# Kernel optimization log

Hardware: AMD Instinct MI355X
Metric: run time of the kernel (lower is better)

## Reference

```python
import jax, jax.numpy as jnp
import numpy as np

N = 50000
E = 800000
FEAT = 128
HID = 128
HEADS = 8
HEAD_DIM = HID // HEADS  # 16
NEG_SLOPE = 0.2


def _gat_layer(x, W, a_src, a_dst, b, src, dst, num_nodes):
    # x: [N, Fin]; W: [Fin, H*C]; a_src/a_dst: [H, C]; b: [H*C]
    H, C = a_src.shape
    h = (x @ W).reshape(num_nodes, H, C)               # [N,H,C]
    alpha_s = jnp.einsum('nhc,hc->nh', h, a_src)       # [N,H]
    alpha_d = jnp.einsum('nhc,hc->nh', h, a_dst)       # [N,H]
    e = jax.nn.leaky_relu(alpha_s[src] + alpha_d[dst], NEG_SLOPE)  # [E,H]
    # segment softmax over destination nodes (every node has a self-loop)
    m = jax.ops.segment_max(e, dst, num_segments=num_nodes)
    e = jnp.exp(e - m[dst])
    s = jax.ops.segment_sum(e, dst, num_segments=num_nodes)
    alpha = e / (s[dst] + 1e-16)                       # [E,H]
    msg = alpha[:, :, None] * h[src]                   # [E,H,C]
    out = jax.ops.segment_sum(msg, dst, num_segments=num_nodes)
    return out.reshape(num_nodes, H * C) + b


def setup_inputs() -> dict:
    key = jax.random.key(0)
    ks = jax.random.split(key, 12)
    x = jax.random.normal(ks[0], (N, FEAT), dtype=jnp.float32)
    edge_index = jax.random.randint(ks[1], (2, E), 0, N, dtype=jnp.int32)
    glorot = lambda k, shape: jax.random.uniform(
        k, shape, jnp.float32,
        -jnp.sqrt(6.0 / (shape[-2] + shape[-1])),
        jnp.sqrt(6.0 / (shape[-2] + shape[-1])))
    W1 = glorot(ks[2], (FEAT, HID))
    a_src1 = glorot(ks[3], (HEADS, HEAD_DIM))
    a_dst1 = glorot(ks[4], (HEADS, HEAD_DIM))
    b1 = jnp.zeros((HID,), jnp.float32)
    W2 = glorot(ks[5], (HID, HID))
    a_src2 = glorot(ks[6], (HEADS, HEAD_DIM))
    a_dst2 = glorot(ks[7], (HEADS, HEAD_DIM))
    b2 = jnp.zeros((HID,), jnp.float32)
    return {"x": x, "edge_index": edge_index,
            "W1": W1, "a_src1": a_src1, "a_dst1": a_dst1, "b1": b1,
            "W2": W2, "a_src2": a_src2, "a_dst2": a_dst2, "b2": b2}


def reference(x, edge_index, W1, a_src1, a_dst1, b1, W2, a_src2, a_dst2, b2):
    # GATConv adds self-loops to the (dense_to_sparse-derived) edge list
    loops = jnp.arange(N, dtype=edge_index.dtype)
    src = jnp.concatenate([edge_index[0], loops])
    dst = jnp.concatenate([edge_index[1], loops])
    h = _gat_layer(x, W1, a_src1, a_dst1, b1, src, dst, N)
    h = jax.nn.elu(h)
    # dropout: inference mode (training=False) -> identity
    h = _gat_layer(h, W2, a_src2, a_dst2, b2, src, dst, N)
    return jax.nn.elu(h)
```

## Files before the change

### kernel.cpp

```cpp
#include <hip/hip_runtime.h>
#include <hip/hip_fp16.h>
#include <math.h>

#define DEGMAX 64
#define CHUNK  2048
#define CAPB   6144

typedef _Float16 half8 __attribute__((ext_vector_type(8)));
typedef float    f32x4 __attribute__((ext_vector_type(4)));

__global__ __launch_bounds__(256) void k_csr(
        const int* __restrict__ gcur, const unsigned* __restrict__ bstore,
        int N, int* __restrict__ cnt, int* __restrict__ offs,
        unsigned short* __restrict__ adj) {
    int b = blockIdx.x;
    int t = threadIdx.x;
    int n0 = b << 8;
    int nb = N - n0; if (nb > 256) nb = 256;
    int ecnt = gcur[b]; if (ecnt > CAPB) ecnt = CAPB;
    __shared__ int lcnt[256], lofs[256], wsum[4];
    __shared__ unsigned short stage[CAPB];
    const unsigned* bp = bstore + (size_t)b * CAPB;

    lcnt[t] = 0;
    __syncthreads();
    for (int i = t; i < ecnt; i += 256)
        atomicAdd(&lcnt[bp[i] >> 16], 1);
    __syncthreads();
    int mycnt = lcnt[t];
    int lane = t & 63, wv = t >> 6;
    int x = mycnt;
    #pragma unroll
    for (int d = 1; d < 64; d <<= 1) {
        int y = __shfl_up(x, d);
        if (lane >= d) x += y;
    }
    if (lane == 63) wsum[wv] = x;
    __syncthreads();
    int base = 0;
    for (int k = 0; k < wv; k++) base += wsum[k];
    int myofs = base + x - mycnt;
    lofs[t] = myofs;
    if (t < nb) {
        cnt[n0 + t]  = mycnt;
        offs[n0 + t] = b * CAPB + myofs;
    }
    __syncthreads();
    lcnt[t] = 0;
    __syncthreads();
    for (int i = t; i < ecnt; i += 256) {
        unsigned p = bp[i];
        int node = p >> 16;
        int r = atomicAdd(&lcnt[node], 1);
        stage[lofs[node] + r] = (unsigned short)(p & 0xffffu);
    }
    __syncthreads();
    for (int i = t; i < ecnt; i += 256)
        adj[(size_t)b * CAPB + i] = stage[i];
}

__global__ void k_wcast(const float* __restrict__ W1, const float* __restrict__ as1,
                        const float* __restrict__ ad1, __half* __restrict__ Wf1,
                        const float* __restrict__ W2, const float* __restrict__ as2,
                        const float* __restrict__ ad2, __half* __restrict__ Wf2,
                        int* __restrict__ gcur) {
    int t = threadIdx.x;
    if (blockIdx.x == 0) gcur[t] = 0;
    int id2 = blockIdx.x * 256 + t;
    if (id2 >= 4608) return;
    int layer = id2 >= 2304 ? 1 : 0;
    const float* W  = layer ? W2  : W1;
    const float* av_s = layer ? as2 : as1;
    const float* av_d = layer ? ad2 : ad1;
    __half* Wf = layer ? Wf2 : Wf1;
    int id = id2 - layer * 2304;
    int lane = id & 63;
    int ct = (id >> 6) % 9;
    int kc = id / 576;
    int q = lane >> 4, n = lane & 15;
    #pragma unroll
    for (int j = 0; j < 8; j++) {
        int k = kc * 32 + q * 8 + j;
        float val;
        if (ct < 8) {
            val = W[(size_t)k * 128 + ct * 16 + n];
        } else {
            int h = n & 7;
            const float* a = (n < 8) ? av_s : av_d;
            float s = 0.f;
            #pragma unroll
            for (int c = 0; c < 16; c++)
                s += W[(size_t)k * 128 + h * 16 + c] * a[h * 16 + c];
            val = s;
        }
        Wf[(size_t)id * 8 + j] = __float2half(val);
    }
}

__device__ inline float4 ld4f(const float* p) { return *(const float4*)p; }

template<typename InT>
__device__ __forceinline__ void gemm_body(
        const InT* __restrict__ X, const __half* __restrict__ Wfrag,
        __half* __restrict__ H16, float* __restrict__ as_out,
        float* __restrict__ ad_out, int M, int bid) {
    __shared__ __half xls[64][136];
    int t = threadIdx.x;
    int w = t >> 6, lane = t & 63;
    int q = lane >> 4, n = lane & 15;
    int row0 = bid * 64;

    half8 bfrag[4][2];
    #pragma unroll
    for (int kc = 0; kc < 4; kc++)
        #pragma unroll
        for (int c2 = 0; c2 < 2; c2++) {
            int ct = w * 2 + c2;
            uint4 u = *(const uint4*)(Wfrag + (((size_t)(kc * 9 + ct)) * 64 + lane) * 8);
            bfrag[kc][c2] = *(half8*)&u;
        }
    half8 bfa[4];
    if (w == 0) {
        #pragma unroll
        for (int kc = 0; kc < 4; kc++) {
            uint4 u = *(const uint4*)(Wfrag + (((size_t)(kc * 9 + 8)) * 64 + lane) * 8);
            bfa[kc] = *(half8*)&u;
        }
    }

    #pragma unroll
    for (int rep = 0; rep < 8; rep++) {
        int lin = rep * 1024 + t * 4;
        int r = lin >> 7, k = lin & 127;
        int gr = row0 + r;
        uint2 u;
        if constexpr (sizeof(InT) == 4) {
            float4 v = (gr < M) ? ld4f((const float*)&X[(size_t)gr * 128 + k])
                                : make_float4(0.f, 0.f, 0.f, 0.f);
            __half2 h0 = __floats2half2_rn(v.x, v.y);
            __half2 h1 = __floats2half2_rn(v.z, v.w);
            u = make_uint2(*(unsigned*)&h0, *(unsigned*)&h1);
        } else {
            u = (gr < M) ? *(const uint2*)&X[(size_t)gr * 128 + k] : make_uint2(0, 0);
        }
        *(uint2*)&xls[r][k] = u;
    }
    __syncthreads();

    f32x4 acc[4][2], acca[4];
    #pragma unroll
    for (int rt = 0; rt < 4; rt++) {
        acc[rt][0] = (f32x4){0.f, 0.f, 0.f, 0.f};
        acc[rt][1] = (f32x4){0.f, 0.f, 0.f, 0.f};
        acca[rt]   = (f32x4){0.f, 0.f, 0.f, 0.f};
    }

    #pragma unroll
    for (int kc = 0; kc < 4; kc++)
        #pragma unroll
        for (int rt = 0; rt < 4; rt++) {
            uint4 au = *(const uint4*)&xls[rt * 16 + n][kc * 32 + q * 8];
            half8 af = *(half8*)&au;
            acc[rt][0] = __builtin_amdgcn_mfma_f32_16x16x32_f16(af, bfrag[kc][0], acc[rt][0], 0, 0, 0);
            acc[rt][1] = __builtin_amdgcn_mfma_f32_16x16x32_f16(af, bfrag[kc][1], acc[rt][1], 0, 0, 0);
            if (w == 0)
                acca[rt] = __builtin_amdgcn_mfma_f32_16x16x32_f16(af, bfa[kc], acca[rt], 0, 0, 0);
        }

    #pragma unroll
    for (int c2 = 0; c2 < 2; c2++) {
        int h = w * 2 + c2;
        #pragma unroll
        for (int rt = 0; rt < 4; rt++)
            #pragma unroll
            for (int reg = 0; reg < 4; reg++) {
                int grow = row0 + rt * 16 + q * 4 + reg;
                if (grow < M)
                    H16[(size_t)grow * 128 + h * 16 + n] = __float2half(acc[rt][c2][reg]);
            }
    }
    if (w == 0) {
        float* aout = (n < 8) ? as_out : ad_out;
        int h = n & 7;
        #pragma unroll
        for (int rt = 0; rt < 4; rt++)
            #pragma unroll
            for (int reg = 0; reg < 4; reg++) {
                int grow = row0 + rt * 16 + q * 4 + reg;
                if (grow < M) aout[grow * 8 + h] = acca[rt][reg];
            }
    }
}

__global__ __launch_bounds__(256) void k_bin_gemm(
        const float* __restrict__ X, const __half* __restrict__ Wfrag,
        __half* __restrict__ H16, float* __restrict__ as_out,
        float* __restrict__ ad_out, int M, int Gg,
        const int* __restrict__ src, const int* __restrict__ dst, int E, int K,
        int* __restrict__ gcur, unsigned* __restrict__ bstore) {
    int bid = blockIdx.x;
    if (bid < Gg) {
        gemm_body<float>(X, Wfrag, H16, as_out, ad_out, M, bid);
        return;
    }
    __shared__ int lcnt[256];
    __shared__ int gbase[256];
    int t = threadIdx.x;
    if (t < K) lcnt[t] = 0;
    __syncthreads();
    int e0 = (bid - Gg) * CHUNK;
    unsigned pk[8]; short bk[8], rk[8];
    #pragma unroll
    for (int j = 0; j < 8; j++) {
        int e = e0 + t + j * 256;
        bool v = e < E;
        int s = v ? src[e] : 0;
        int d = v ? dst[e] : 0;
        int b = d >> 8;
        pk[j] = ((unsigned)(d & 255) << 16) | (unsigned)s;
        bk[j] = (short)b;
        rk[j] = v ? (short)atomicAdd(&lcnt[b], 1) : (short)-1;
    }
    __syncthreads();
    if (t < K) gbase[t] = lcnt[t] ? atomicAdd(&gcur[t], lcnt[t]) : 0;
    __syncthreads();
    #pragma unroll
    for (int j = 0; j < 8; j++) {
        if (rk[j] >= 0) {
            int b = bk[j];
            int pos = gbase[b] + rk[j];
            if (pos < CAPB) bstore[(size_t)b * CAPB + pos] = pk[j];
        }
    }
}

__global__ __launch_bounds__(256) void k_gemm_mfma_h(
        const __half* __restrict__ X, const __half* __restrict__ Wfrag,
        __half* __restrict__ H16, float* __restrict__ as_out,
        float* __restrict__ ad_out, int M) {
    gemm_body<__half>(X, Wfrag, H16, as_out, ad_out, M, blockIdx.x);
}

#define LOADB(ii, LG, HR)                                                     \
    {                                                                         \
        int e_ = (ii) + (lane >> 3);                                          \
        int se_ = __shfl(sv, (e_ < deg) ? e_ : 0);                            \
        LG = as_[(size_t)se_ * 8 + (lane & 7)];                               \
        _Pragma("unroll")                                                     \
        for (int j_ = 0; j_ < 8; j_++) {                                      \
            int idx_ = (ii) + j_; if (idx_ >= deg) idx_ = deg - 1;            \
            int sj_ = __shfl(sv, idx_);                                       \
            HR[j_] = *(const unsigned*)&H[(size_t)sj_ * 128 + lane * 2];      \
        }                                                                     \
    }

#define COMPB(ii, LG, HR)                                                     \
    {                                                                         \
        float v_ = LG + adv;                                                  \
        v_ = v_ > 0.f ? v_ : 0.2f * v_;                                       \
        float wgt_ = ((ii) + (lane >> 3) < deg) ? __expf(v_) : 0.f;           \
        _Pragma("unroll")                                                     \
        for (int j_ = 0; j_ < 8; j_++) {                                      \
            float wj_ = __shfl(wgt_, j_ * 8 + hd);                            \
            float2 hv_ = __half22float2(*(__half2*)&HR[j_]);                  \
            ssum += wj_; ax += wj_ * hv_.x; ay += wj_ * hv_.y;                \
        }                                                                     \
    }

template<typename OutT>
__global__ __launch_bounds__(256) void k_aggregate(
        const __half* __restrict__ H, const float* __restrict__ as_,
        const float* __restrict__ ad_, const int* __restrict__ cnt,
        const int* __restrict__ offs, const unsigned short* __restrict__ adj,
        const float* __restrict__ bias, OutT* __restrict__ out, int N) {
    int wave = (int)((blockIdx.x * blockDim.x + threadIdx.x) >> 6);
    int lane = threadIdx.x & 63;
    if (wave >= N) return;
    int n = wave;
    int hd = lane >> 3;
    int deg = cnt[n]; if (deg > DEGMAX) deg = DEGMAX;
    int row = offs[n];
    int sv = (lane < deg) ? (int)adj[row + lane] : n;
    float adv = ad_[n * 8 + (lane & 7)];

    float vs = as_[n * 8 + hd] + ad_[n * 8 + hd];
    vs = vs > 0.f ? vs : 0.2f * vs;
    float wsf = __expf(vs);
    unsigned hrs = *(const unsigned*)&H[(size_t)n * 128 + lane * 2];
    float2 hvs = __half22float2(*(__half2*)&hrs);
    float ssum = wsf, ax = wsf * hvs.x, ay = wsf * hvs.y;

    float lg0, lg1, lg2, lg3;
    unsigned hr0[8], hr1[8], hr2[8], hr3[8];
    if (deg > 0)  LOADB(0,  lg0, hr0);
    if (deg > 8)  LOADB(8,  lg1, hr1);
    if (deg > 16) LOADB(16, lg2, hr2);
    if (deg > 24) LOADB(24, lg3, hr3);
    if (deg > 0)  COMPB(0,  lg0, hr0);
    if (deg > 8)  COMPB(8,  lg1, hr1);
    if (deg > 16) COMPB(16, lg2, hr2);
    if (deg > 24) COMPB(24, lg3, hr3);
    for (int i = 32; i < deg; i += 8) {
        float lgt; unsigned hrt[8];
        LOADB(i, lgt, hrt);
        COMPB(i, lgt, hrt);
    }

    float inv = 1.f / (ssum + 1e-16f);
    float ox = ax * inv + bias[lane * 2];
    float oy = ay * inv + bias[lane * 2 + 1];
    ox = ox > 0.f ? ox : __expf(ox) - 1.f;
    oy = oy > 0.f ? oy : __expf(oy) - 1.f;
    if constexpr (sizeof(OutT) == 2) {
        __half2 hv = __floats2half2_rn(ox, oy);
        *(__half2*)&out[(size_t)n * 128 + lane * 2] = hv;
    } else {
        *(float2*)&out[(size_t)n * 128 + lane * 2] = make_float2(ox, oy);
    }
}

static inline char* bump(char*& w, size_t bytes) {
    char* p = w;
    w += (bytes + 255) & ~(size_t)255;
    return p;
}

extern "C" void kernel_launch(void* const* d_in, const int* in_sizes, int n_in,
                              void* d_out, int out_size, void* d_ws, size_t ws_size,
                              hipStream_t stream) {
    const float* x   = (const float*)d_in[0];
    const int*   ei  = (const int*)d_in[1];
    const float* W1  = (const float*)d_in[2];
    const float* as1 = (const float*)d_in[3];
    const float* ad1 = (const float*)d_in[4];
    const float* b1  = (const float*)d_in[5];
    const float* W2  = (const float*)d_in[6];
    const float* as2 = (const float*)d_in[7];
    const float* ad2 = (const float*)d_in[8];
    const float* b2  = (const float*)d_in[9];
    float* out = (float*)d_out;

    int N = in_sizes[0] / 128;
    int E = in_sizes[1] / 2;
    const int* srcs = ei;
    const int* dsts = ei + E;
    int K = (N + 255) >> 8;
    int Gg = (N + 63) / 64;
    int Bb = (E + CHUNK - 1) / CHUNK;

    char* w = (char*)d_ws;
    int*            cnt   = (int*)           bump(w, (size_t)N * sizeof(int));
    int*            offs  = (int*)           bump(w, (size_t)N * sizeof(int));
    int*            gcur  = (int*)           bump(w, 256 * sizeof(int));
    unsigned*       bst   = (unsigned*)      bump(w, (size_t)256 * CAPB * sizeof(unsigned));
    unsigned short* adj   = (unsigned short*)bump(w, (size_t)256 * CAPB * sizeof(unsigned short));
    __half*         H16   = (__half*)        bump(w, (size_t)N * 128 * sizeof(__half));
    __half*         A16   = (__half*)        bump(w, (size_t)N * 128 * sizeof(__half));
    float*          asb   = (float*)         bump(w, (size_t)N * 8 * sizeof(float));
    float*          adb   = (float*)         bump(w, (size_t)N * 8 * sizeof(float));
    __half*         Wf1   = (__half*)        bump(w, 18432 * sizeof(__half));
    __half*         Wf2   = (__half*)        bump(w, 18432 * sizeof(__half));

    k_wcast<<<18, 256, 0, stream>>>(W1, as1, ad1, Wf1, W2, as2, ad2, Wf2, gcur);
    k_bin_gemm<<<Gg + Bb, 256, 0, stream>>>(x, Wf1, H16, asb, adb, N, Gg,
                                            srcs, dsts, E, K, gcur, bst);
    k_csr<<<K, 256, 0, stream>>>(gcur, bst, N, cnt, offs, adj);
    k_aggregate<__half><<<(N + 3) / 4, 256, 0, stream>>>(H16, asb, adb, cnt, offs, adj, b1, A16, N);
    k_gemm_mfma_h<<<Gg, 256, 0, stream>>>(A16, Wf2, H16, asb, adb, N);
    k_aggregate<float><<<(N + 3) / 4, 256, 0, stream>>>(H16, asb, adb, cnt, offs, adj, b2, out, N);
}
```

Measured before the change: 218.0 us.

## Use 16-byte neighbor row gathers with cross-lane reduction in GAT aggregate

Changes the aggregate kernel's lane mapping so each lane loads 8 halfs (uint4) of a neighbor row. Four edges are handled per wave per load instead of each lane loading 4 bytes for every edge. Partial sums across edge groups are then combined with xor-shuffles, and only 16 lanes finalize and store 16-byte outputs. The aim is fewer, wider gather instructions and fewer shuffles per edge. In exchange it adds a final reduction and leaves 48 lanes idle in the epilogue.

```diff
diff --git a/kernel.cpp b/kernel.cpp
--- a/kernel.cpp
+++ b/kernel.cpp
@@ -241,29 +241,44 @@
     gemm_body<__half>(X, Wfrag, H16, as_out, ad_out, M, blockIdx.x);
 }
 
-#define LOADB(ii, LG, HR)                                                     \
+#define LOADW(ii, LG)                                                         \
     {                                                                         \
-        int e_ = (ii) + (lane >> 3);                                          \
+        int e_ = (ii) + es;                                                   \
         int se_ = __shfl(sv, (e_ < deg) ? e_ : 0);                            \
-        LG = as_[(size_t)se_ * 8 + (lane & 7)];                               \
-        _Pragma("unroll")                                                     \
-        for (int j_ = 0; j_ < 8; j_++) {                                      \
-            int idx_ = (ii) + j_; if (idx_ >= deg) idx_ = deg - 1;            \
-            int sj_ = __shfl(sv, idx_);                                       \
-            HR[j_] = *(const unsigned*)&H[(size_t)sj_ * 128 + lane * 2];      \
-        }                                                                     \
-    }
-
-#define COMPB(ii, LG, HR)                                                     \
+        LG = as_[(size_t)se_ * 8 + h8];                                       \
+    }
+
+#define LOADH(ii, U0, U1)                                                     \
+    {                                                                         \
+        int i0_ = (ii) + g;     if (i0_ >= deg) i0_ = deg - 1;                \
+        int s0_ = __shfl(sv, i0_);                                            \
+        U0 = *(const uint4*)&H[(size_t)s0_ * 128 + f0];                       \
+        int i1_ = (ii) + 4 + g; if (i1_ >= deg) i1_ = deg - 1;                \
+        int s1_ = __shfl(sv, i1_);                                            \
+        U1 = *(const uint4*)&H[(size_t)s1_ * 128 + f0];                       \
+    }
+
+#define COMP(ii, LG, U0, U1)                                                  \
     {                                                                         \
         float v_ = LG + adv;                                                  \
         v_ = v_ > 0.f ? v_ : 0.2f * v_;                                       \
-        float wgt_ = ((ii) + (lane >> 3) < deg) ? __expf(v_) : 0.f;           \
+        float w_ = ((ii) + es < deg) ? __expf(v_) : 0.f;                      \
+        ssA += w_;                                                            \
+        float wj0_ = __shfl(w_, g * 8 + hf);                                  \
+        const __half2* hp0_ = (const __half2*)&U0;                            \
         _Pragma("unroll")                                                     \
-        for (int j_ = 0; j_ < 8; j_++) {                                      \
-            float wj_ = __shfl(wgt_, j_ * 8 + hd);                            \
-            float2 hv_ = __half22float2(*(__half2*)&HR[j_]);                  \
-            ssum += wj_; ax += wj_ * hv_.x; ay += wj_ * hv_.y;                \
+        for (int k_ = 0; k_ < 4; k_++) {                                      \
+            float2 f_ = __half22float2(hp0_[k_]);                             \
+            acc[2 * k_]     += wj0_ * f_.x;                                   \
+            acc[2 * k_ + 1] += wj0_ * f_.y;                                   \
+        }                                                                     \
+        float wj1_ = __shfl(w_, (4 + g) * 8 + hf);                            \
+        const __half2* hp1_ = (const __half2*)&U1;                            \
+        _Pragma("unroll")                                                     \
+        for (int k_ = 0; k_ < 4; k_++) {                                      \
+            float2 f_ = __half22float2(hp1_[k_]);                             \
+            acc[2 * k_]     += wj1_ * f_.x;                                   \
+            acc[2 * k_ + 1] += wj1_ * f_.y;                                   \
         }                                                                     \
     }
 
@@ -277,45 +292,79 @@
     int lane = threadIdx.x & 63;
     if (wave >= N) return;
     int n = wave;
-    int hd = lane >> 3;
+    int es = lane >> 3, h8 = lane & 7;
+    int g = lane >> 4;
+    int f0 = (lane & 15) * 8;
+    int hf = (lane & 15) >> 1;
     int deg = cnt[n]; if (deg > DEGMAX) deg = DEGMAX;
     int row = offs[n];
     int sv = (lane < deg) ? (int)adj[row + lane] : n;
-    float adv = ad_[n * 8 + (lane & 7)];
-
-    float vs = as_[n * 8 + hd] + ad_[n * 8 + hd];
-    vs = vs > 0.f ? vs : 0.2f * vs;
-    float wsf = __expf(vs);
-    unsigned hrs = *(const unsigned*)&H[(size_t)n * 128 + lane * 2];
-    float2 hvs = __half22float2(*(__half2*)&hrs);
-    float ssum = wsf, ax = wsf * hvs.x, ay = wsf * hvs.y;
+
+    float adv = ad_[n * 8 + h8];
+    float asv = as_[n * 8 + h8];
+    float vsl = asv + adv;
+    vsl = vsl > 0.f ? vsl : 0.2f * vsl;
+    float wsf = __expf(vsl);
+    float ssA = (es == 0) ? wsf : 0.f;
+
+    float acc[8];
+    #pragma unroll
+    for (int k = 0; k < 8; k++) acc[k] = 0.f;
 
     float lg0, lg1, lg2, lg3;
-    unsigned hr0[8], hr1[8], hr2[8], hr3[8];
-    if (deg > 0)  LOADB(0,  lg0, hr0);
-    if (deg > 8)  LOADB(8,  lg1, hr1);
-    if (deg > 16) LOADB(16, lg2, hr2);
-    if (deg > 24) LOADB(24, lg3, hr3);
-    if (deg > 0)  COMPB(0,  lg0, hr0);
-    if (deg > 8)  COMPB(8,  lg1, hr1);
-    if (deg > 16) COMPB(16, lg2, hr2);
-    if (deg > 24) COMPB(24, lg3, hr3);
+    uint4 a0, b0, a1, b1, a2, b2, a3, b3;
+    if (deg > 0)  { LOADW(0,  lg0); LOADH(0,  a0, b0); }
+    if (deg > 8)  { LOADW(8,  lg1); LOADH(8,  a1, b1); }
+    if (deg > 16) { LOADW(16, lg2); LOADH(16, a2, b2); }
+    if (deg > 24) { LOADW(24, lg3); LOADH(24, a3, b3); }
+    if (deg > 0)  COMP(0,  lg0, a0, b0);
+    if (deg > 8)  COMP(8,  lg1, a1, b1);
+    if (deg > 16) COMP(16, lg2, a2, b2);
+    if (deg > 24) COMP(24, lg3, a3, b3);
     for (int i = 32; i < deg; i += 8) {
-        float lgt; unsigned hrt[8];
-        LOADB(i, lgt, hrt);
-        COMPB(i, lgt, hrt);
-    }
-
-    float inv = 1.f / (ssum + 1e-16f);
-    float ox = ax * inv + bias[lane * 2];
-    float oy = ay * inv + bias[lane * 2 + 1];
-    ox = ox > 0.f ? ox : __expf(ox) - 1.f;
-    oy = oy > 0.f ? oy : __expf(oy) - 1.f;
-    if constexpr (sizeof(OutT) == 2) {
-        __half2 hv = __floats2half2_rn(ox, oy);
-        *(__half2*)&out[(size_t)n * 128 + lane * 2] = hv;
-    } else {
-        *(float2*)&out[(size_t)n * 128 + lane * 2] = make_float2(ox, oy);
+        float lgt; uint4 u0, u1;
+        LOADW(i, lgt); LOADH(i, u0, u1);
+        COMP(i, lgt, u0, u1);
+    }
+
+    #pragma unroll
+    for (int k = 0; k < 8; k++) {
+        acc[k] += __shfl_xor(acc[k], 16);
+        acc[k] += __shfl_xor(acc[k], 32);
+    }
+    ssA += __shfl_xor(ssA, 8);
+    ssA += __shfl_xor(ssA, 16);
+    ssA += __shfl_xor(ssA, 32);
+    float ssum = __shfl(ssA, hf);
+    float wsb  = __shfl(wsf, hf);
+    uint4 hs = *(const uint4*)&H[(size_t)n * 128 + f0];
+
+    if (lane < 16) {
+        const __half2* hp = (const __half2*)&hs;
+        float inv = 1.f / (ssum + 1e-16f);
+        float o[8];
+        #pragma unroll
+        for (int k = 0; k < 4; k++) {
+            float2 f2 = __half22float2(hp[k]);
+            o[2 * k]     = (acc[2 * k]     + wsb * f2.x) * inv;
+            o[2 * k + 1] = (acc[2 * k + 1] + wsb * f2.y) * inv;
+        }
+        float4 bv0 = *(const float4*)&bias[f0];
+        float4 bv1 = *(const float4*)&bias[f0 + 4];
+        o[0] += bv0.x; o[1] += bv0.y; o[2] += bv0.z; o[3] += bv0.w;
+        o[4] += bv1.x; o[5] += bv1.y; o[6] += bv1.z; o[7] += bv1.w;
+        #pragma unroll
+        for (int k = 0; k < 8; k++)
+            o[k] = o[k] > 0.f ? o[k] : __expf(o[k]) - 1.f;
+        if constexpr (sizeof(OutT) == 2) {
+            __half2 p[4];
+            #pragma unroll
+            for (int k = 0; k < 4; k++) p[k] = __floats2half2_rn(o[2 * k], o[2 * k + 1]);
+            *(uint4*)&out[(size_t)n * 128 + f0] = *(uint4*)p;
+        } else {
+            *(float4*)&out[(size_t)n * 128 + f0]     = make_float4(o[0], o[1], o[2], o[3]);
+            *(float4*)&out[(size_t)n * 128 + f0 + 4] = make_float4(o[4], o[5], o[6], o[7]);
+        }
     }
 }
 
```

New measurement: 221.8 us. Within noise of the previous version (+1.7%).

## Fuse layer-1 aggregation with layer-2 GEMM in one kernel

Applied to the files above, without the earlier changes.

Layer-1 aggregation and the layer-2 projection GEMM now run in a single 512-thread kernel. Each block aggregates 64 nodes (8 waves × 8 nodes), stages the fp16 results in LDS, then runs MFMA with W2 to write H16b plus the attention logits. This drops the A16 round trip through global memory and one kernel launch. In exchange the aggregation goes from one node per wave across many blocks to 8 serial nodes per wave, which lowers latency-hiding parallelism in the gather-heavy phase. Separate H16b/asb2/adb2 buffers avoid overwriting layer-1 data that other blocks are still reading.

```diff
diff --git a/kernel.cpp b/kernel.cpp
--- a/kernel.cpp
+++ b/kernel.cpp
@@ -99,9 +99,8 @@
 
 __device__ inline float4 ld4f(const float* p) { return *(const float4*)p; }
 
-template<typename InT>
-__device__ __forceinline__ void gemm_body(
-        const InT* __restrict__ X, const __half* __restrict__ Wfrag,
+__device__ __forceinline__ void gemm_body_f32(
+        const float* __restrict__ X, const __half* __restrict__ Wfrag,
         __half* __restrict__ H16, float* __restrict__ as_out,
         float* __restrict__ ad_out, int M, int bid) {
     __shared__ __half xls[64][136];
@@ -133,16 +132,11 @@
         int lin = rep * 1024 + t * 4;
         int r = lin >> 7, k = lin & 127;
         int gr = row0 + r;
-        uint2 u;
-        if constexpr (sizeof(InT) == 4) {
-            float4 v = (gr < M) ? ld4f((const float*)&X[(size_t)gr * 128 + k])
-                                : make_float4(0.f, 0.f, 0.f, 0.f);
-            __half2 h0 = __floats2half2_rn(v.x, v.y);
-            __half2 h1 = __floats2half2_rn(v.z, v.w);
-            u = make_uint2(*(unsigned*)&h0, *(unsigned*)&h1);
-        } else {
-            u = (gr < M) ? *(const uint2*)&X[(size_t)gr * 128 + k] : make_uint2(0, 0);
-        }
+        float4 v = (gr < M) ? ld4f(&X[(size_t)gr * 128 + k])
+                            : make_float4(0.f, 0.f, 0.f, 0.f);
+        __half2 h0 = __floats2half2_rn(v.x, v.y);
+        __half2 h1 = __floats2half2_rn(v.z, v.w);
+        uint2 u = make_uint2(*(unsigned*)&h0, *(unsigned*)&h1);
         *(uint2*)&xls[r][k] = u;
     }
     __syncthreads();
@@ -154,7 +148,6 @@
         acc[rt][1] = (f32x4){0.f, 0.f, 0.f, 0.f};
         acca[rt]   = (f32x4){0.f, 0.f, 0.f, 0.f};
     }
-
     #pragma unroll
     for (int kc = 0; kc < 4; kc++)
         #pragma unroll
@@ -200,7 +193,7 @@
         int* __restrict__ gcur, unsigned* __restrict__ bstore) {
     int bid = blockIdx.x;
     if (bid < Gg) {
-        gemm_body<float>(X, Wfrag, H16, as_out, ad_out, M, bid);
+        gemm_body_f32(X, Wfrag, H16, as_out, ad_out, M, bid);
         return;
     }
     __shared__ int lcnt[256];
@@ -232,13 +225,6 @@
             if (pos < CAPB) bstore[(size_t)b * CAPB + pos] = pk[j];
         }
     }
-}
-
-__global__ __launch_bounds__(256) void k_gemm_mfma_h(
-        const __half* __restrict__ X, const __half* __restrict__ Wfrag,
-        __half* __restrict__ H16, float* __restrict__ as_out,
-        float* __restrict__ ad_out, int M) {
-    gemm_body<__half>(X, Wfrag, H16, as_out, ad_out, M, blockIdx.x);
 }
 
 #define LOADB(ii, LG, HR)                                                     \
@@ -267,16 +253,11 @@
         }                                                                     \
     }
 
-template<typename OutT>
-__global__ __launch_bounds__(256) void k_aggregate(
+__device__ __forceinline__ float2 agg_node(
         const __half* __restrict__ H, const float* __restrict__ as_,
         const float* __restrict__ ad_, const int* __restrict__ cnt,
         const int* __restrict__ offs, const unsigned short* __restrict__ adj,
-        const float* __restrict__ bias, OutT* __restrict__ out, int N) {
-    int wave = (int)((blockIdx.x * blockDim.x + threadIdx.x) >> 6);
-    int lane = threadIdx.x & 63;
-    if (wave >= N) return;
-    int n = wave;
+        const float* __restrict__ bias, int n, int lane) {
     int hd = lane >> 3;
     int deg = cnt[n]; if (deg > DEGMAX) deg = DEGMAX;
     int row = offs[n];
@@ -311,12 +292,98 @@
     float oy = ay * inv + bias[lane * 2 + 1];
     ox = ox > 0.f ? ox : __expf(ox) - 1.f;
     oy = oy > 0.f ? oy : __expf(oy) - 1.f;
-    if constexpr (sizeof(OutT) == 2) {
-        __half2 hv = __floats2half2_rn(ox, oy);
-        *(__half2*)&out[(size_t)n * 128 + lane * 2] = hv;
-    } else {
-        *(float2*)&out[(size_t)n * 128 + lane * 2] = make_float2(ox, oy);
-    }
+    return make_float2(ox, oy);
+}
+
+__global__ __launch_bounds__(512) void k_agg_gemm(
+        const __half* __restrict__ H, const float* __restrict__ as_,
+        const float* __restrict__ ad_, const int* __restrict__ cnt,
+        const int* __restrict__ offs, const unsigned short* __restrict__ adj,
+        const float* __restrict__ bias, const __half* __restrict__ Wfrag,
+        __half* __restrict__ H16b, float* __restrict__ as2,
+        float* __restrict__ ad2, int N) {
+    __shared__ __half xls[64][136];
+    int t = threadIdx.x;
+    int w = t >> 6, lane = t & 63;
+    int q = lane >> 4, nn = lane & 15;
+    int row0 = blockIdx.x * 64;
+
+    half8 bf[4];
+    #pragma unroll
+    for (int kc = 0; kc < 4; kc++) {
+        uint4 u = *(const uint4*)(Wfrag + (((size_t)(kc * 9 + w)) * 64 + lane) * 8);
+        bf[kc] = *(half8*)&u;
+    }
+    half8 bfa[4];
+    if (w == 0) {
+        #pragma unroll
+        for (int kc = 0; kc < 4; kc++) {
+            uint4 u = *(const uint4*)(Wfrag + (((size_t)(kc * 9 + 8)) * 64 + lane) * 8);
+            bfa[kc] = *(half8*)&u;
+        }
+    }
+
+    for (int i = 0; i < 8; i++) {
+        int r = w * 8 + i;
+        int n = row0 + r;
+        __half2 hv;
+        if (n < N) {
+            float2 o = agg_node(H, as_, ad_, cnt, offs, adj, bias, n, lane);
+            hv = __floats2half2_rn(o.x, o.y);
+        } else {
+            hv = __floats2half2_rn(0.f, 0.f);
+        }
+        *(__half2*)&xls[r][lane * 2] = hv;
+    }
+    __syncthreads();
+
+    f32x4 acc[4], acca[4];
+    #pragma unroll
+    for (int rt = 0; rt < 4; rt++) {
+        acc[rt]  = (f32x4){0.f, 0.f, 0.f, 0.f};
+        acca[rt] = (f32x4){0.f, 0.f, 0.f, 0.f};
+    }
+    #pragma unroll
+    for (int kc = 0; kc < 4; kc++)
+        #pragma unroll
+        for (int rt = 0; rt < 4; rt++) {
+            uint4 au = *(const uint4*)&xls[rt * 16 + nn][kc * 32 + q * 8];
+            half8 af = *(half8*)&au;
+            acc[rt] = __builtin_amdgcn_mfma_f32_16x16x32_f16(af, bf[kc], acc[rt], 0, 0, 0);
+            if (w == 0)
+                acca[rt] = __builtin_amdgcn_mfma_f32_16x16x32_f16(af, bfa[kc], acca[rt], 0, 0, 0);
+        }
+    #pragma unroll
+    for (int rt = 0; rt < 4; rt++)
+        #pragma unroll
+        for (int reg = 0; reg < 4; reg++) {
+            int grow = row0 + rt * 16 + q * 4 + reg;
+            if (grow < N)
+                H16b[(size_t)grow * 128 + w * 16 + nn] = __float2half(acc[rt][reg]);
+        }
+    if (w == 0) {
+        float* aout = (nn < 8) ? as2 : ad2;
+        int h = nn & 7;
+        #pragma unroll
+        for (int rt = 0; rt < 4; rt++)
+            #pragma unroll
+            for (int reg = 0; reg < 4; reg++) {
+                int grow = row0 + rt * 16 + q * 4 + reg;
+                if (grow < N) aout[grow * 8 + h] = acca[rt][reg];
+            }
+    }
+}
+
+__global__ __launch_bounds__(256) void k_aggregate_f(
+        const __half* __restrict__ H, const float* __restrict__ as_,
+        const float* __restrict__ ad_, const int* __restrict__ cnt,
+        const int* __restrict__ offs, const unsigned short* __restrict__ adj,
+        const float* __restrict__ bias, float* __restrict__ out, int N) {
+    int wave = (int)((blockIdx.x * blockDim.x + threadIdx.x) >> 6);
+    int lane = threadIdx.x & 63;
+    if (wave >= N) return;
+    float2 o = agg_node(H, as_, ad_, cnt, offs, adj, bias, wave, lane);
+    *(float2*)&out[(size_t)wave * 128 + lane * 2] = o;
 }
 
 static inline char* bump(char*& w, size_t bytes) {
@@ -355,9 +422,11 @@
     unsigned*       bst   = (unsigned*)      bump(w, (size_t)256 * CAPB * sizeof(unsigned));
     unsigned short* adj   = (unsigned short*)bump(w, (size_t)256 * CAPB * sizeof(unsigned short));
     __half*         H16   = (__half*)        bump(w, (size_t)N * 128 * sizeof(__half));
-    __half*         A16   = (__half*)        bump(w, (size_t)N * 128 * sizeof(__half));
+    __half*         H16b  = (__half*)        bump(w, (size_t)N * 128 * sizeof(__half));
     float*          asb   = (float*)         bump(w, (size_t)N * 8 * sizeof(float));
     float*          adb   = (float*)         bump(w, (size_t)N * 8 * sizeof(float));
+    float*          asb2  = (float*)         bump(w, (size_t)N * 8 * sizeof(float));
+    float*          adb2  = (float*)         bump(w, (size_t)N * 8 * sizeof(float));
     __half*         Wf1   = (__half*)        bump(w, 18432 * sizeof(__half));
     __half*         Wf2   = (__half*)        bump(w, 18432 * sizeof(__half));
 
@@ -365,7 +434,8 @@
     k_bin_gemm<<<Gg + Bb, 256, 0, stream>>>(x, Wf1, H16, asb, adb, N, Gg,
                                             srcs, dsts, E, K, gcur, bst);
     k_csr<<<K, 256, 0, stream>>>(gcur, bst, N, cnt, offs, adj);
-    k_aggregate<__half><<<(N + 3) / 4, 256, 0, stream>>>(H16, asb, adb, cnt, offs, adj, b1, A16, N);
-    k_gemm_mfma_h<<<Gg, 256, 0, stream>>>(A16, Wf2, H16, asb, adb, N);
-    k_aggregate<float><<<(N + 3) / 4, 256, 0, stream>>>(H16, asb, adb, cnt, offs, adj, b2, out, N);
-}
+    k_agg_gemm<<<Gg, 512, 0, stream>>>(H16, asb, adb, cnt, offs, adj, b1, Wf2,
+                                       H16b, asb2, adb2, N);
+    k_aggregate_f<<<(N + 3) / 4, 256, 0, stream>>>(H16b, asb2, adb2, cnt, offs,
+                                                   adj, b2, out, N);
+}
```

After: 257.6 us. +18.1%, slower.
